# Kernel optimization log

Hardware: AMD Instinct MI355X
Metric: run time of the kernel (lower is better)

Reference implementation:

```python
import jax, jax.numpy as jnp
import numpy as np

H = 16  # n_heads
D = 64  # d_keys


def setup_inputs() -> dict:
    key = jax.random.key(0)
    ks = jax.random.split(key, 11)
    b, n, dm = 2, 2048, 1024
    s = 1.0 / np.sqrt(dm)
    return {
        "q": jax.random.normal(ks[0], (b, n, dm), jnp.float32),
        "k": jax.random.normal(ks[1], (b, n, dm), jnp.float32),
        "v": jax.random.normal(ks[2], (b, n, dm), jnp.float32),
        "Wq": jax.random.normal(ks[3], (dm, H * D), jnp.float32) * s,
        "bq": jax.random.normal(ks[4], (H * D,), jnp.float32) * 0.01,
        "Wk": jax.random.normal(ks[5], (dm, H * D), jnp.float32) * s,
        "bk": jax.random.normal(ks[6], (H * D,), jnp.float32) * 0.01,
        "Wv": jax.random.normal(ks[7], (dm, H * D), jnp.float32) * s,
        "bv": jax.random.normal(ks[8], (H * D,), jnp.float32) * 0.01,
        "Wo": jax.random.normal(ks[9], (H * D, dm), jnp.float32) * s,
        "bo": jax.random.normal(ks[10], (dm,), jnp.float32) * 0.01,
    }


def reference(q, k, v, Wq, bq, Wk, bk, Wv, bv, Wo, bo):
    b, n_q, _ = q.shape
    n_k = k.shape[1]
    # projections -> [b, n, h, d]
    qh = (q @ Wq + bq).reshape(b, n_q, H, D)
    kh = (k @ Wk + bk).reshape(b, n_k, H, D)
    vh = (v @ Wv + bv).reshape(b, n_k, H, D)
    # scores [b, h, n, m]
    scores = jnp.einsum('bnhd,bmhd->bhnm', qh, kh)
    causal = jnp.triu(jnp.ones((n_q, n_k), dtype=bool), k=1)  # True above diag
    scores = jnp.where(causal, -jnp.inf, scores)
    att = jax.nn.softmax(scores / np.sqrt(D).astype(np.float32), axis=-1)
    att_out = jnp.einsum('bhnm,bmhd->bnhd', att, vh).reshape(b, n_q, H * D)
    return att_out @ Wo + bo
```

## Files before the change

### kernel.cpp

```cpp
#include <hip/hip_runtime.h>

typedef float f32x4 __attribute__((ext_vector_type(4)));
typedef __bf16 bf16x8 __attribute__((ext_vector_type(8)));
typedef __bf16 bf16x4 __attribute__((ext_vector_type(4)));
typedef __bf16 bf16_t;

#define NH 16
#define DH 64
#define SEQ 2048
#define DM 1024

#define QSCALE 0.18033688f

extern "C" hipError_t hipMemPtrGetInfo(void* ptr, size_t* size);

__device__ __forceinline__ bf16x8 ld8(const bf16_t* p) { return *(const bf16x8*)p; }
__device__ __forceinline__ void st8(bf16_t* p, bf16x8 v) { *(bf16x8*)p = v; }

__device__ __forceinline__ void gl_lds16(const bf16_t* g, bf16_t* l)
{
    __builtin_amdgcn_global_load_lds(
        (const __attribute__((address_space(1))) unsigned int*)g,
        (__attribute__((address_space(3))) unsigned int*)l, 16, 0, 0);
}

__global__ __launch_bounds__(256) void fill_sentinel(float* out, unsigned n, float val)
{
    unsigned stride = gridDim.x * blockDim.x;
    for (unsigned i = blockIdx.x * blockDim.x + threadIdx.x; i < n; i += stride)
        out[i] = val;
}

__global__ __launch_bounds__(256) void prep(
    const float* __restrict__ q, const float* __restrict__ k,
    const float* __restrict__ v,
    const float* __restrict__ w0, const float* __restrict__ w1,
    const float* __restrict__ w2, const float* __restrict__ w3,
    bf16_t* __restrict__ xb, bf16_t* __restrict__ wt, int fragmode)
{
    int z = blockIdx.z;
    if (z < 3) {
        const float* src = (z == 0) ? q : (z == 1) ? k : v;
        bf16_t* dst = xb + (size_t)z * (4096u * 1024u);
        size_t i8 = ((size_t)blockIdx.x * 256 + threadIdx.x) * 8;
        f32x4 u = *(const f32x4*)(src + i8);
        f32x4 w = *(const f32x4*)(src + i8 + 4);
        bf16x8 h = { (bf16_t)u.x, (bf16_t)u.y, (bf16_t)u.z, (bf16_t)u.w,
                     (bf16_t)w.x, (bf16_t)w.y, (bf16_t)w.z, (bf16_t)w.w };
        st8(dst + i8, h);
    } else {
        int x = blockIdx.x;
        if (x >= 1024) return;
        int w = x >> 8, rem = x & 255;
        int bx = rem & 15, by = rem >> 4;
        const float* in = (w == 0) ? w0 : (w == 1) ? w1 : (w == 2) ? w2 : w3;
        bf16_t* out = wt + (size_t)w * DM * DM;
        __shared__ __align__(16) bf16_t tile[64][72];
        int t = threadIdx.x;
        int k0 = by * 64, n0 = bx * 64;
        int r0 = t >> 4, c0 = (t & 15) * 4;
        for (int p = 0; p < 4; p++) {
            int r = r0 + p * 16;
            const float* src = in + (size_t)(k0 + r) * DM + n0 + c0;
            for (int i = 0; i < 4; i++) tile[r][c0 + i] = (bf16_t)src[i];
        }
        __syncthreads();
        if (fragmode && w < 3) {
            int idx = t;
            #pragma unroll
            for (int p = 0; p < 2; p++, idx += 256) {
                int rn = idx & 63;
                int kc8 = idx >> 6;
                int n_abs = n0 + rn;
                int rblk = n_abs >> 4, l16v = n_abs & 15;
                int kk = kc8 >> 2, gg = kc8 & 3;
                bf16x8 vv;
                for (int j = 0; j < 8; j++) vv[j] = tile[kc8 * 8 + j][rn];
                st8(out + (size_t)((rblk * 16 + by) * 2 + kk) * 512
                        + (gg * 16 + l16v) * 8, vv);
            }
        } else {
            for (int p = 0; p < 4; p++) {
                int rn = r0 + p * 16;
                bf16_t* dst = out + (size_t)(n0 + rn) * DM + k0 + c0;
                for (int i = 0; i < 4; i++) dst[i] = tile[c0 + i][rn];
            }
        }
    }
}

#define LGKM0 asm volatile("s_waitcnt lgkmcnt(0)" ::: "memory")
#define VMC(n) asm volatile("s_waitcnt vmcnt(" #n ")" ::: "memory")
#define BARRIER __builtin_amdgcn_s_barrier()

#define STA(d, h, dk) do { \
    _Pragma("unroll") for (int j = 0; j < 2; j++) \
        gl_lds16(Xp + ((h) * 128 + j * 64) * DM + (dk) * 64, \
                 Ab + sdst0 + ((d) * 2 + (h)) * 8192 + j * 4096); } while (0)
#define RDA(d, h, F) do { \
    _Pragma("unroll") for (int mf = 0; mf < 4; mf++) { \
        F[mf][0] = ld8(Ab + rA0 + ((d) * 2 + (h)) * 8192 + mf * 1024); \
        F[mf][1] = ld8(Ab + rA1 + ((d) * 2 + (h)) * 8192 + mf * 1024); } } while (0)
#define LDB(SET, nh, kto) do { \
    _Pragma("unroll") for (int nf = 0; nf < 2; nf++) \
        _Pragma("unroll") for (int kk = 0; kk < 2; kk++) \
            SET[nf][kk] = ld8(Bp + (nh) * 131072 + nf * 16384 \
                              + (kto) * 1024 + kk * 512); } while (0)
#define MMQ(AF, BF, Q) do { \
    __builtin_amdgcn_s_setprio(1); \
    _Pragma("unroll") for (int mf = 0; mf < 4; mf++) \
        _Pragma("unroll") for (int nf = 0; nf < 2; nf++) { \
            Q[mf][nf] = __builtin_amdgcn_mfma_f32_16x16x32_bf16( \
                AF[mf][0], BF[nf][0], Q[mf][nf], 0, 0, 0); \
            Q[mf][nf] = __builtin_amdgcn_mfma_f32_16x16x32_bf16( \
                AF[mf][1], BF[nf][1], Q[mf][nf], 0, 0, 0); } \
    __builtin_amdgcn_s_setprio(0); } while (0)

__global__ __launch_bounds__(512, 2) void gemm8(
    const bf16_t* __restrict__ xall, const bf16_t* __restrict__ bfall,
    const float* __restrict__ b0v, const float* __restrict__ b1v,
    const float* __restrict__ b2v, bf16_t* __restrict__ outall)
{
    int z = blockIdx.z;
    int mode = z;
    const bf16_t* X  = xall  + (size_t)z * (4096u * 1024u);
    const bf16_t* Bf = bfall + (size_t)z * (1024u * 1024u);
    const float* bias = (z == 0) ? b0v : (z == 1) ? b1v : b2v;
    bf16_t* out = outall + (size_t)z * (4096u * 1024u);

    int m0 = blockIdx.x * 256;
    int n0 = blockIdx.y * 256;

    __shared__ __align__(16) bf16_t Ab[2 * 2 * 128 * 64];

    int tid  = threadIdx.x;
    int lane = tid & 63, w = tid >> 6;
    int g = lane >> 4, l16 = lane & 15;
    int wm = w >> 2, wn = w & 3;
    int rl = lane >> 3, cl = lane & 7;
    int w8 = w * 8;

    int srow = w8 + rl;
    int scol = (cl ^ rl) * 8;
    const bf16_t* Xp = X + (size_t)(m0 + srow) * DM + scol;
    int sdst0 = w8 * 64 + lane * 8;

    int x7 = l16 & 7;
    int rA0 = (wm * 64 + l16) * 64 + ((0 + g) ^ x7) * 8;
    int rA1 = (wm * 64 + l16) * 64 + ((4 + g) ^ x7) * 8;

    const bf16_t* Bp = Bf + ((size_t)(n0 >> 4) + wn * 2) * 16384 + lane * 8;

    f32x4 a00[4][2] = {}, a01[4][2] = {}, a10[4][2] = {}, a11[4][2] = {};
    bf16x8 afA[4][2], afB[4][2], Ba[2][2], Bb[2][2];

    STA(0, 0, 0); STA(0, 1, 0); STA(1, 0, 1); STA(1, 1, 1);
    LDB(Ba, 0, 0); LDB(Bb, 1, 0);
    VMC(0);
    BARRIER;
    RDA(0, 0, afA);

    #pragma unroll 1
    for (int i = 0; i < 7; i++) {
        VMC(6); LGKM0; MMQ(afA, Ba, a00); BARRIER;
        STA(0, 0, 2); VMC(4); RDA(0, 1, afB); MMQ(afA, Bb, a01); BARRIER;
        LGKM0; MMQ(afB, Ba, a10); LDB(Ba, 0, 1); BARRIER;
        MMQ(afB, Bb, a11); LDB(Bb, 1, 1); STA(0, 1, 2); RDA(1, 0, afA); BARRIER;
        VMC(6); LGKM0; MMQ(afA, Ba, a00); BARRIER;
        STA(1, 0, 3); VMC(4); RDA(1, 1, afB); MMQ(afA, Bb, a01); BARRIER;
        LGKM0; MMQ(afB, Ba, a10); LDB(Ba, 0, 2); BARRIER;
        MMQ(afB, Bb, a11); LDB(Bb, 1, 2); STA(1, 1, 3); RDA(0, 0, afA); BARRIER;
        Xp += 128; Bp += 2048;
    }
    VMC(6); LGKM0; MMQ(afA, Ba, a00); BARRIER;
    VMC(2); RDA(0, 1, afB); MMQ(afA, Bb, a01); BARRIER;
    LGKM0; MMQ(afB, Ba, a10); LDB(Ba, 0, 1); BARRIER;
    MMQ(afB, Bb, a11); LDB(Bb, 1, 1); RDA(1, 0, afA); BARRIER;
    VMC(4); LGKM0; MMQ(afA, Ba, a00); BARRIER;
    VMC(0); RDA(1, 1, afB); MMQ(afA, Bb, a01); BARRIER;
    LGKM0; MMQ(afB, Ba, a10); BARRIER;
    MMQ(afB, Bb, a11);

    float scale = (mode == 0) ? QSCALE : 1.0f;
#define EPI(Q, Mh, Nh) do { \
    _Pragma("unroll") for (int mf = 0; mf < 4; mf++) { \
        int mbase = m0 + (Mh) * 128 + wm * 64 + mf * 16 + g * 4; \
        int bb = mbase >> 11, nn0 = mbase & 2047; \
        _Pragma("unroll") for (int nf = 0; nf < 2; nf++) { \
            int col = n0 + (Nh) * 128 + wn * 32 + nf * 16 + l16; \
            float bv = bias[col]; \
            int hh = col >> 6, dd = col & 63; \
            if (mode == 2) { \
                bf16x4 pv; \
                for (int r = 0; r < 4; r++) pv[r] = (bf16_t)(Q[mf][nf][r] + bv); \
                *(bf16x4*)(out + ((size_t)(bb * NH + hh) * DH + dd) * SEQ + nn0) = pv; \
            } else { \
                for (int r = 0; r < 4; r++) \
                    out[((size_t)(bb * NH + hh) * SEQ + nn0 + r) * DH + dd] = \
                        (bf16_t)((Q[mf][nf][r] + bv) * scale); \
            } } } } while (0)
    EPI(a00, 0, 0); EPI(a01, 0, 1); EPI(a10, 1, 0); EPI(a11, 1, 1);
#undef EPI
}

__global__ __launch_bounds__(256) void gemm_out(
    const bf16_t* __restrict__ X, const bf16_t* __restrict__ WT,
    const float* __restrict__ bias, bf16_t* __restrict__ out,
    float* __restrict__ outf, int out_is_f32)
{
    int m0 = blockIdx.x * 128;
    int n0 = blockIdx.y * 128;

    __shared__ __align__(16) bf16_t Alds[128 * 64];
    __shared__ __align__(16) bf16_t Blds[128 * 64];

    int t = threadIdx.x;
    int lane = t & 63, wave = t >> 6;
    int g = lane >> 4, l16 = lane & 15;
    int wr0 = (wave >> 1) * 64, wc0 = (wave & 1) * 64;
    int crow = lane >> 3;
    int ccol = (lane & 7) * 8;

    f32x4 acc[4][4] = {};

    for (int k0 = 0; k0 < DM; k0 += 64) {
        __syncthreads();
        for (int c = wave; c < 16; c += 4) {
            int row = c * 8 + crow;
            gl_lds16(X  + (size_t)(m0 + row) * DM + k0 + ccol,
                     Alds + c * 512 + lane * 8);
            gl_lds16(WT + (size_t)(n0 + row) * DM + k0 + ccol,
                     Blds + c * 512 + lane * 8);
        }
        __syncthreads();
        for (int kk = 0; kk < 2; kk++) {
            bf16x8 af[4], bfr[4];
            for (int i = 0; i < 4; i++)
                af[i] = ld8(Alds + (wr0 + i * 16 + l16) * 64 + kk * 32 + g * 8);
            for (int i = 0; i < 4; i++)
                bfr[i] = ld8(Blds + (wc0 + i * 16 + l16) * 64 + kk * 32 + g * 8);
            for (int mi = 0; mi < 4; mi++)
                for (int ni = 0; ni < 4; ni++)
                    acc[mi][ni] = __builtin_amdgcn_mfma_f32_16x16x32_bf16(
                        af[mi], bfr[ni], acc[mi][ni], 0, 0, 0);
        }
    }
    for (int mi = 0; mi < 4; mi++) {
        int mbase = m0 + wr0 + mi * 16 + g * 4;
        for (int ni = 0; ni < 4; ni++) {
            int col = n0 + wc0 + ni * 16 + l16;
            float bv = bias[col];
            for (int r = 0; r < 4; r++) {
                float sv = acc[mi][ni][r] + bv;
                if (out_is_f32) outf[(size_t)(mbase + r) * 1024 + col] = sv;
                else            out[(size_t)(mbase + r) * 1024 + col] = (bf16_t)sv;
            }
        }
    }
}

__global__ __launch_bounds__(256) void gemm_mha(
    const float* __restrict__ x0, const float* __restrict__ x1,
    const float* __restrict__ x2, const bf16_t* __restrict__ xb,
    const bf16_t* __restrict__ wt_base,
    const float* __restrict__ b0, const float* __restrict__ b1,
    const float* __restrict__ b2, bf16_t* __restrict__ out_base,
    float* __restrict__ outf, int mode_base, int out_is_f32)
{
    int z = blockIdx.z;
    const float* Xf    = (z == 0) ? x0 : (z == 1) ? x1 : x2;
    const bf16_t* WT   = wt_base + (size_t)z * DM * DM;
    const float* bias  = (z == 0) ? b0 : (z == 1) ? b1 : b2;
    bf16_t* out = out_base + (size_t)z * (4096u * 1024u);
    int mode = mode_base + z;

    int m0 = blockIdx.x * 128;
    int n0 = blockIdx.y * 128;

    __shared__ __align__(16) bf16_t Alds[128 * 64];
    __shared__ __align__(16) bf16_t Blds[128 * 64];

    int t = threadIdx.x;
    int lane = t & 63, wave = t >> 6;
    int g = lane >> 4, l16 = lane & 15;
    int wr0 = (wave >> 1) * 64, wc0 = (wave & 1) * 64;

    f32x4 acc[4][4] = {};
    int srow = t >> 3, sk = (t & 7) * 8;

    for (int k0 = 0; k0 < DM; k0 += 64) {
        __syncthreads();
        if (mode < 3) {
            for (int p = 0; p < 4; p++) {
                int r = srow + p * 32;
                const float* s4 = Xf + (size_t)(m0 + r) * DM + k0 + sk;
                f32x4 u = *(const f32x4*)s4;
                f32x4 w = *(const f32x4*)(s4 + 4);
                bf16x8 h = { (bf16_t)u.x, (bf16_t)u.y, (bf16_t)u.z, (bf16_t)u.w,
                             (bf16_t)w.x, (bf16_t)w.y, (bf16_t)w.z, (bf16_t)w.w };
                st8(Alds + r * 64 + sk, h);
            }
        } else {
            for (int p = 0; p < 4; p++) {
                int r = srow + p * 32;
                st8(Alds + r * 64 + sk, ld8(xb + (size_t)(m0 + r) * DM + k0 + sk));
            }
        }
        for (int p = 0; p < 4; p++) {
            int r = srow + p * 32;
            st8(Blds + r * 64 + sk, ld8(WT + (size_t)(n0 + r) * DM + k0 + sk));
        }
        __syncthreads();
        for (int kk = 0; kk < 2; kk++) {
            bf16x8 af[4], bfr[4];
            for (int i = 0; i < 4; i++)
                af[i] = ld8(Alds + (wr0 + i * 16 + l16) * 64 + kk * 32 + g * 8);
            for (int i = 0; i < 4; i++)
                bfr[i] = ld8(Blds + (wc0 + i * 16 + l16) * 64 + kk * 32 + g * 8);
            for (int mi = 0; mi < 4; mi++)
                for (int ni = 0; ni < 4; ni++)
                    acc[mi][ni] = __builtin_amdgcn_mfma_f32_16x16x32_bf16(
                        af[mi], bfr[ni], acc[mi][ni], 0, 0, 0);
        }
    }
    float scale = (mode == 0) ? QSCALE : 1.0f;
    for (int mi = 0; mi < 4; mi++) {
        int mbase = m0 + wr0 + mi * 16 + g * 4;
        for (int ni = 0; ni < 4; ni++) {
            int col = n0 + wc0 + ni * 16 + l16;
            float bv = bias[col];
            if (mode == 2) {
                int bb = mbase >> 11, nn0 = mbase & 2047;
                int h = col >> 6, d = col & 63;
                bf16x4 pv;
                for (int r = 0; r < 4; r++) pv[r] = (bf16_t)(acc[mi][ni][r] + bv);
                *(bf16x4*)(out + ((size_t)(bb * NH + h) * DH + d) * SEQ + nn0) = pv;
            } else {
                for (int r = 0; r < 4; r++) {
                    int mr = mbase + r;
                    float sv = (acc[mi][ni][r] + bv) * scale;
                    if (mode == 3) {
                        if (out_is_f32) outf[(size_t)mr * 1024 + col] = sv;
                        else            out[(size_t)mr * 1024 + col] = (bf16_t)sv;
                    } else {
                        int bb = mr >> 11, nn = mr & 2047;
                        int h = col >> 6, d = col & 63;
                        out[((size_t)(bb * NH + h) * SEQ + nn) * DH + d] = (bf16_t)sv;
                    }
                }
            }
        }
    }
}

__constant__ unsigned char JP[24] = {7,15,15,14,14,6,13,13,12,12,5,11,
                                     11,10,10,4,9,9,8,8,3,2,1,0};
__constant__ unsigned char JS[24] = {0,0,1,0,1,0,0,1,0,1,0,0,
                                     1,0,1,0,0,1,0,1,0,0,0,0};

__global__ __launch_bounds__(512) void attn_split(
    const bf16_t* __restrict__ Qh, const bf16_t* __restrict__ Kh,
    const bf16_t* __restrict__ VT, bf16_t* __restrict__ att,
    float* __restrict__ Pb, float* __restrict__ Lb)
{
    int bhx = blockIdx.x;
    int y   = blockIdx.y;
    int p   = JP[y];
    int seg = JS[y];
    bool splitf = (p >= 8);
    int k0 = splitf ? seg * (p + 1) : 0;
    int k1 = splitf ? k0 + (p + 1) : 2 * p + 2;

    const bf16_t* Qb = Qh + (size_t)bhx * SEQ * DH;
    const bf16_t* Kb = Kh + (size_t)bhx * SEQ * DH;
    const bf16_t* Vb = VT + (size_t)bhx * DH * SEQ;

    __shared__ __align__(16) bf16_t Klds[2][64 * 72];
    __shared__ __align__(16) bf16_t Vlds[2][64 * 72];
    __shared__ __align__(16) bf16_t Plds[8][16 * 72];

    int t = threadIdx.x, lane = t & 63, wave = t >> 6;
    int g = lane >> 4, l16 = lane & 15;
    int srow = t >> 3, sk = (t & 7) * 8;
    int qt = 2 * p + (wave >> 2);
    int Tw = qt + 1;
    int rowl = (wave & 3) * 16 + l16;

    bf16x8 qf[2];
    for (int kk = 0; kk < 2; kk++)
        qf[kk] = ld8(Qb + (size_t)(qt * 64 + rowl) * DH + kk * 32 + g * 8);

    f32x4 accO[4] = {};
    float l = 0.f;
    bf16_t* Pw = Plds[wave];

    st8(&Klds[0][srow * 72 + sk], ld8(Kb + (size_t)(k0 * 64 + srow) * DH + sk));
    st8(&Vlds[0][srow * 72 + sk], ld8(Vb + (size_t)srow * SEQ + k0 * 64 + sk));

    for (int j = k0; j < k1; j++) {
        __syncthreads();
        bool pre = (j + 1 < k1);
        bf16x8 kreg, vreg;
        if (pre) {
            kreg = ld8(Kb + (size_t)((j + 1) * 64 + srow) * DH + sk);
            vreg = ld8(Vb + (size_t)srow * SEQ + (j + 1) * 64 + sk);
        }
        if (j < Tw) {
            int buf = (j - k0) & 1;
            bool diag = (j == Tw - 1);

            f32x4 s[4];
            __builtin_amdgcn_s_setprio(1);
            for (int c = 0; c < 4; c++) {
                f32x4 a = {};
                for (int kk = 0; kk < 2; kk++) {
                    bf16x8 kf = ld8(&Klds[buf][(c * 16 + l16) * 72 + kk * 32 + g * 8]);
                    a = __builtin_amdgcn_mfma_f32_16x16x32_bf16(kf, qf[kk], a, 0, 0, 0);
                }
                s[c] = a;
            }
            __builtin_amdgcn_s_setprio(0);
            for (int c = 0; c < 4; c++) {
                bf16x4 pv;
                for (int r = 0; r < 4; r++) {
                    float v = s[c][r];
                    if (diag && (c * 16 + g * 4 + r) > rowl) v = -1e30f;
                    float pe;
                    asm("v_exp_f32 %0, %1" : "=v"(pe) : "v"(v));
                    l += pe;
                    pv[r] = (bf16_t)pe;
                }
                *(bf16x4*)(Pw + l16 * 72 + c * 16 + g * 4) = pv;
            }
            asm volatile("s_waitcnt lgkmcnt(0)" ::: "memory");

            bf16x8 pf0 = ld8(Pw + l16 * 72 + g * 8);
            bf16x8 pf1 = ld8(Pw + l16 * 72 + 32 + g * 8);
            __builtin_amdgcn_s_setprio(1);
            for (int c2 = 0; c2 < 4; c2++) {
                bf16x8 vf0 = ld8(&Vlds[buf][(c2 * 16 + l16) * 72 + g * 8]);
                accO[c2] = __builtin_amdgcn_mfma_f32_16x16x32_bf16(vf0, pf0, accO[c2], 0, 0, 0);
                bf16x8 vf1 = ld8(&Vlds[buf][(c2 * 16 + l16) * 72 + 32 + g * 8]);
                accO[c2] = __builtin_amdgcn_mfma_f32_16x16x32_bf16(vf1, pf1, accO[c2], 0, 0, 0);
            }
            __builtin_amdgcn_s_setprio(0);

            if (diag && !splitf) {
                float lt = l;
                lt += __shfl_xor(lt, 16);
                lt += __shfl_xor(lt, 32);
                float inv = 1.f / lt;
                int qabs = qt * 64 + rowl;
                int bb = bhx >> 4, h = bhx & 15;
                for (int c2 = 0; c2 < 4; c2++) {
                    bf16x4 ov;
                    for (int r = 0; r < 4; r++) ov[r] = (bf16_t)(accO[c2][r] * inv);
                    *(bf16x4*)(att + (((size_t)bb * SEQ + qabs) * NH + h) * DH
                               + c2 * 16 + g * 4) = ov;
                }
            }
        }
        if (pre) {
            int b = (j - k0 + 1) & 1;
            st8(&Klds[b][srow * 72 + sk], kreg);
            st8(&Vlds[b][srow * 72 + sk], vreg);
        }
    }

    if (splitf) {
        float lt = l;
        lt += __shfl_xor(lt, 16);
        lt += __shfl_xor(lt, 32);
        int slot = (bhx * 16 + (qt - 16)) * 2 + seg;
        float* Pp = Pb + (size_t)slot * 4096 + rowl * 64;
        #pragma unroll
        for (int c2 = 0; c2 < 4; c2++)
            *(f32x4*)(Pp + c2 * 16 + g * 4) = accO[c2];
        if (g == 0) Lb[slot * 64 + rowl] = lt;
    }
}

__global__ __launch_bounds__(256) void attn_combine(
    const float* __restrict__ Pb, const float* __restrict__ Lb,
    bf16_t* __restrict__ att)
{
    int bhx = blockIdx.x, q16 = blockIdx.y;
    int qt = 16 + q16;
    int t = threadIdx.x;
    int row = t >> 2, dc = (t & 3) * 16;

    int slot0 = (bhx * 16 + q16) * 2;
    int slot1 = slot0 + 1;
    float lsum = Lb[slot0 * 64 + row] + Lb[slot1 * 64 + row];
    float inv = 1.f / lsum;

    const float* P0 = Pb + (size_t)slot0 * 4096 + row * 64 + dc;
    const float* P1 = Pb + (size_t)slot1 * 4096 + row * 64 + dc;
    int qabs = qt * 64 + row;
    int bb = bhx >> 4, h = bhx & 15;
    bf16_t* ob = att + (((size_t)bb * SEQ + qabs) * NH + h) * DH + dc;
    #pragma unroll
    for (int c = 0; c < 4; c++) {
        f32x4 a = *(const f32x4*)(P0 + c * 4);
        f32x4 b = *(const f32x4*)(P1 + c * 4);
        bf16x4 ov;
        for (int r = 0; r < 4; r++) ov[r] = (bf16_t)((a[r] + b[r]) * inv);
        *(bf16x4*)(ob + c * 4) = ov;
    }
}

__global__ __launch_bounds__(512) void attn(
    const bf16_t* __restrict__ Qh, const bf16_t* __restrict__ Kh,
    const bf16_t* __restrict__ VT, bf16_t* __restrict__ att)
{
    int bhx = blockIdx.x;
    int yy  = blockIdx.y;
    int p   = (yy < 8) ? yy : 23 - yy;
    int TB  = 2 * p + 2;

    const bf16_t* Qb = Qh + (size_t)bhx * SEQ * DH;
    const bf16_t* Kb = Kh + (size_t)bhx * SEQ * DH;
    const bf16_t* Vb = VT + (size_t)bhx * DH * SEQ;

    __shared__ __align__(16) bf16_t Klds[2][64 * 72];
    __shared__ __align__(16) bf16_t Vlds[2][64 * 72];
    __shared__ __align__(16) bf16_t Plds[8][16 * 72];

    int t = threadIdx.x, lane = t & 63, wave = t >> 6;
    int g = lane >> 4, l16 = lane & 15;
    int srow = t >> 3, sk = (t & 7) * 8;
    int qt = 2 * p + (wave >> 2);
    int Tw = qt + 1;
    int rowl = (wave & 3) * 16 + l16;

    bf16x8 qf[2];
    for (int kk = 0; kk < 2; kk++)
        qf[kk] = ld8(Qb + (size_t)(qt * 64 + rowl) * DH + kk * 32 + g * 8);

    f32x4 accO[4] = {};
    float l = 0.f;
    bf16_t* Pw = Plds[wave];

    st8(&Klds[0][srow * 72 + sk], ld8(Kb + (size_t)srow * DH + sk));
    st8(&Vlds[0][srow * 72 + sk], ld8(Vb + (size_t)srow * SEQ + sk));

    for (int j = 0; j < TB; j++) {
        __syncthreads();
        bool pre = (j + 1 < TB);
        bf16x8 kreg, vreg;
        if (pre) {
            kreg = ld8(Kb + (size_t)((j + 1) * 64 + srow) * DH + sk);
            vreg = ld8(Vb + (size_t)srow * SEQ + (j + 1) * 64 + sk);
        }
        if (j < Tw) {
            int buf = j & 1;
            bool diag = (j == Tw - 1);

            f32x4 s[4];
            __builtin_amdgcn_s_setprio(1);
            for (int c = 0; c < 4; c++) {
                f32x4 a = {};
                for (int kk = 0; kk < 2; kk++) {
                    bf16x8 kf = ld8(&Klds[buf][(c * 16 + l16) * 72 + kk * 32 + g * 8]);
                    a = __builtin_amdgcn_mfma_f32_16x16x32_bf16(kf, qf[kk], a, 0, 0, 0);
                }
                s[c] = a;
            }
            __builtin_amdgcn_s_setprio(0);
            for (int c = 0; c < 4; c++) {
                bf16x4 pv;
                for (int r = 0; r < 4; r++) {
                    float v = s[c][r];
                    if (diag && (c * 16 + g * 4 + r) > rowl) v = -1e30f;
                    float pe;
                    asm("v_exp_f32 %0, %1" : "=v"(pe) : "v"(v));
                    l += pe;
                    pv[r] = (bf16_t)pe;
                }
                *(bf16x4*)(Pw + l16 * 72 + c * 16 + g * 4) = pv;
            }
            asm volatile("s_waitcnt lgkmcnt(0)" ::: "memory");

            bf16x8 pf0 = ld8(Pw + l16 * 72 + g * 8);
            bf16x8 pf1 = ld8(Pw + l16 * 72 + 32 + g * 8);
            __builtin_amdgcn_s_setprio(1);
            for (int c2 = 0; c2 < 4; c2++) {
                bf16x8 vf0 = ld8(&Vlds[buf][(c2 * 16 + l16) * 72 + g * 8]);
                accO[c2] = __builtin_amdgcn_mfma_f32_16x16x32_bf16(vf0, pf0, accO[c2], 0, 0, 0);
                bf16x8 vf1 = ld8(&Vlds[buf][(c2 * 16 + l16) * 72 + 32 + g * 8]);
                accO[c2] = __builtin_amdgcn_mfma_f32_16x16x32_bf16(vf1, pf1, accO[c2], 0, 0, 0);
            }
            __builtin_amdgcn_s_setprio(0);

            if (diag) {
                float lt = l;
                lt += __shfl_xor(lt, 16);
                lt += __shfl_xor(lt, 32);
                float inv = 1.f / lt;
                int qabs = qt * 64 + rowl;
                int bb = bhx >> 4, h = bhx & 15;
                for (int c2 = 0; c2 < 4; c2++) {
                    bf16x4 ov;
                    for (int r = 0; r < 4; r++) ov[r] = (bf16_t)(accO[c2][r] * inv);
                    *(bf16x4*)(att + (((size_t)bb * SEQ + qabs) * NH + h) * DH
                               + c2 * 16 + g * 4) = ov;
                }
            }
        }
        if (pre) {
            int b = (j + 1) & 1;
            st8(&Klds[b][srow * 72 + sk], kreg);
            st8(&Vlds[b][srow * 72 + sk], vreg);
        }
    }
}

extern "C" void kernel_launch(void* const* d_in, const int* in_sizes, int n_in,
                              void* d_out, int out_size, void* d_ws, size_t ws_size,
                              hipStream_t stream) {
    const float* q  = (const float*)d_in[0];
    const float* k  = (const float*)d_in[1];
    const float* v  = (const float*)d_in[2];
    const float* Wq = (const float*)d_in[3];
    const float* bq = (const float*)d_in[4];
    const float* Wk = (const float*)d_in[5];
    const float* bk = (const float*)d_in[6];
    const float* Wv = (const float*)d_in[7];
    const float* bv = (const float*)d_in[8];
    const float* Wo = (const float*)d_in[9];
    const float* bo = (const float*)d_in[10];

    const size_t MAT = 1024u * 1024u;
    const size_t BIG = 4096u * 1024u;
    const size_t NEED_BASE = 64 + (4 * BIG + 4 * MAT) * 2;
    const size_t NEED_FAST = NEED_BASE + 3 * BIG * 2;

    if (ws_size < NEED_BASE) {
        fill_sentinel<<<1024, 256, 0, stream>>>((float*)d_out,
                                                (unsigned)out_size, 100.0f);
        return;
    }

    int out_is_f32 = 1;
    size_t osz = 0;
    if (hipMemPtrGetInfo(d_out, &osz) == hipSuccess && osz != 0 &&
        osz < (size_t)out_size * 4)
        out_is_f32 = 0;

    bf16_t* base = (bf16_t*)d_ws + 32;
    bf16_t* Qh  = base;
    bf16_t* Kh  = Qh + BIG;
    bf16_t* VT  = Kh + BIG;
    bf16_t* att = VT + BIG;
    bf16_t* WT  = att + BIG;
    bf16_t* Xb  = WT + 4 * MAT;

    if (ws_size >= NEED_FAST) {
        float* Pb = (float*)Xb;
        float* Lb = Pb + (size_t)1024 * 4096;
        prep<<<dim3(2048, 1, 4), 256, 0, stream>>>(q, k, v, Wq, Wk, Wv, Wo,
                                                   Xb, WT, 1);
        gemm8<<<dim3(16, 4, 3), 512, 0, stream>>>(Xb, WT, bq, bk, bv, Qh);
        attn_split<<<dim3(32, 24), 512, 0, stream>>>(Qh, Kh, VT, att, Pb, Lb);
        attn_combine<<<dim3(32, 16), 256, 0, stream>>>(Pb, Lb, att);
        gemm_out<<<dim3(32, 8), 256, 0, stream>>>(att, WT + 3 * MAT, bo,
                                                  (bf16_t*)d_out, (float*)d_out,
                                                  out_is_f32);
    } else {
        prep<<<dim3(2048, 1, 4), 256, 0, stream>>>(q, k, v, Wq, Wk, Wv, Wo,
                                                   (bf16_t*)d_ws, WT, 0);
        gemm_mha<<<dim3(32, 8, 3), 256, 0, stream>>>(q, k, v, nullptr, WT,
                                                     bq, bk, bv, Qh, nullptr, 0, 0);
        attn<<<dim3(32, 16), 512, 0, stream>>>(Qh, Kh, VT, att);
        gemm_mha<<<dim3(32, 8, 1), 256, 0, stream>>>(nullptr, nullptr, nullptr, att,
                                                     WT + 3 * MAT, bo, bo, bo,
                                                     (bf16_t*)d_out, (float*)d_out,
                                                     3, out_is_f32);
    }
}
```

Baseline: 227.5 us.

## Single-buffer K/V LDS in attention with staggered register prefetch and extra barrier

Replaces double-buffered K and V shared-memory tiles with single buffers. Register prefetch is staggered so V is stored at the loop top and K is stored after a new mid-iteration barrier, once the QK^T phase has finished reading it. This halves the LDS footprint for K/V, which could allow more blocks per CU. In exchange it adds a second __syncthreads per iteration and prefetches K two tiles ahead.

```diff
diff --git a/kernel.cpp b/kernel.cpp
--- a/kernel.cpp
+++ b/kernel.cpp
@@ -375,8 +375,8 @@
     const bf16_t* Kb = Kh + (size_t)bhx * SEQ * DH;
     const bf16_t* Vb = VT + (size_t)bhx * DH * SEQ;
 
-    __shared__ __align__(16) bf16_t Klds[2][64 * 72];
-    __shared__ __align__(16) bf16_t Vlds[2][64 * 72];
+    __shared__ __align__(16) bf16_t Klds[64 * 72];
+    __shared__ __align__(16) bf16_t Vlds[64 * 72];
     __shared__ __align__(16) bf16_t Plds[8][16 * 72];
 
     int t = threadIdx.x, lane = t & 63, wave = t >> 6;
@@ -394,27 +394,27 @@
     float l = 0.f;
     bf16_t* Pw = Plds[wave];
 
-    st8(&Klds[0][srow * 72 + sk], ld8(Kb + (size_t)(k0 * 64 + srow) * DH + sk));
-    st8(&Vlds[0][srow * 72 + sk], ld8(Vb + (size_t)srow * SEQ + k0 * 64 + sk));
+    bf16x8 kreg = ld8(Kb + (size_t)(k0 * 64 + srow) * DH + sk);
+    bf16x8 vreg = ld8(Vb + (size_t)srow * SEQ + k0 * 64 + sk);
+    st8(&Klds[srow * 72 + sk], kreg);
+    if (k0 + 1 < k1)
+        kreg = ld8(Kb + (size_t)((k0 + 1) * 64 + srow) * DH + sk);
 
     for (int j = k0; j < k1; j++) {
         __syncthreads();
-        bool pre = (j + 1 < k1);
-        bf16x8 kreg, vreg;
-        if (pre) {
-            kreg = ld8(Kb + (size_t)((j + 1) * 64 + srow) * DH + sk);
+        st8(&Vlds[srow * 72 + sk], vreg);
+        if (j + 1 < k1)
             vreg = ld8(Vb + (size_t)srow * SEQ + (j + 1) * 64 + sk);
-        }
-        if (j < Tw) {
-            int buf = (j - k0) & 1;
-            bool diag = (j == Tw - 1);
-
+
+        bool act  = (j < Tw);
+        bool diag = (j == Tw - 1);
+        if (act) {
             f32x4 s[4];
             __builtin_amdgcn_s_setprio(1);
             for (int c = 0; c < 4; c++) {
                 f32x4 a = {};
                 for (int kk = 0; kk < 2; kk++) {
-                    bf16x8 kf = ld8(&Klds[buf][(c * 16 + l16) * 72 + kk * 32 + g * 8]);
+                    bf16x8 kf = ld8(&Klds[(c * 16 + l16) * 72 + kk * 32 + g * 8]);
                     a = __builtin_amdgcn_mfma_f32_16x16x32_bf16(kf, qf[kk], a, 0, 0, 0);
                 }
                 s[c] = a;
@@ -432,15 +432,21 @@
                 }
                 *(bf16x4*)(Pw + l16 * 72 + c * 16 + g * 4) = pv;
             }
-            asm volatile("s_waitcnt lgkmcnt(0)" ::: "memory");
-
+        }
+        __syncthreads();
+        if (j + 1 < k1) {
+            st8(&Klds[srow * 72 + sk], kreg);
+            if (j + 2 < k1)
+                kreg = ld8(Kb + (size_t)((j + 2) * 64 + srow) * DH + sk);
+        }
+        if (act) {
             bf16x8 pf0 = ld8(Pw + l16 * 72 + g * 8);
             bf16x8 pf1 = ld8(Pw + l16 * 72 + 32 + g * 8);
             __builtin_amdgcn_s_setprio(1);
             for (int c2 = 0; c2 < 4; c2++) {
-                bf16x8 vf0 = ld8(&Vlds[buf][(c2 * 16 + l16) * 72 + g * 8]);
+                bf16x8 vf0 = ld8(&Vlds[(c2 * 16 + l16) * 72 + g * 8]);
                 accO[c2] = __builtin_amdgcn_mfma_f32_16x16x32_bf16(vf0, pf0, accO[c2], 0, 0, 0);
-                bf16x8 vf1 = ld8(&Vlds[buf][(c2 * 16 + l16) * 72 + 32 + g * 8]);
+                bf16x8 vf1 = ld8(&Vlds[(c2 * 16 + l16) * 72 + 32 + g * 8]);
                 accO[c2] = __builtin_amdgcn_mfma_f32_16x16x32_bf16(vf1, pf1, accO[c2], 0, 0, 0);
             }
             __builtin_amdgcn_s_setprio(0);
@@ -459,11 +465,6 @@
                                + c2 * 16 + g * 4) = ov;
                 }
             }
-        }
-        if (pre) {
-            int b = (j - k0 + 1) & 1;
-            st8(&Klds[b][srow * 72 + sk], kreg);
-            st8(&Vlds[b][srow * 72 + sk], vreg);
         }
     }
 
```

Result: no change. 225.9 us (-0.7%).
